# Performance work log

Measured on AMD Instinct MI355X. Metric: run time of the kernel, lower is better.

The kernel has to match this reference:

```python
import jax, jax.numpy as jnp
import numpy as np

N = 100000      # num nodes
E = 1600000     # random edges
F_IN = 128      # n_features
H1, H2 = 128, 64   # gnns_forward_hidden
FC1, C = 128, 10   # linears_hidden[-1], n_classes
M = 20000       # masked nodes
SLOPE = 0.2     # LeakyReLU negative slope (GATConv default)


def _glorot(key, shape):
    fan = shape[0]
    return jax.random.normal(key, shape, dtype=jnp.float32) / jnp.sqrt(jnp.float32(fan))


def setup_inputs() -> dict:
    key = jax.random.key(0)
    ks = jax.random.split(key, 16)
    x = jax.random.normal(ks[0], (N, F_IN), dtype=jnp.float32)
    edge_index = jax.random.randint(ks[1], (2, E), 0, N, dtype=jnp.int64)
    mask = jax.random.randint(ks[2], (M,), 0, N, dtype=jnp.int64)
    return {
        "x": x, "edge_index": edge_index, "mask": mask,
        # GAT layer 1: F_IN -> H1
        "W1": _glorot(ks[3], (F_IN, H1)),
        "a_src1": _glorot(ks[4], (H1,)), "a_dst1": _glorot(ks[5], (H1,)),
        "b1": jnp.zeros((H1,), jnp.float32),
        # GAT layer 2: H1 -> H2
        "W2": _glorot(ks[6], (H1, H2)),
        "a_src2": _glorot(ks[7], (H2,)), "a_dst2": _glorot(ks[8], (H2,)),
        "b2": jnp.zeros((H2,), jnp.float32),
        # FC head: H2 -> FC1 -> C
        "fc1_w": _glorot(ks[9], (H2, FC1)), "fc1_b": jnp.zeros((FC1,), jnp.float32),
        "fc2_w": _glorot(ks[10], (FC1, C)), "fc2_b": jnp.zeros((C,), jnp.float32),
    }


def _gat_layer(x, src, dst, W, a_src, a_dst, b):
    h = x @ W                                   # [N, F_out]
    alpha_s = h @ a_src                         # [N]
    alpha_d = h @ a_dst                         # [N]
    e = jax.nn.leaky_relu(alpha_s[src] + alpha_d[dst], SLOPE)  # [E+N]
    # segment softmax over incoming edges of each destination node
    m = jax.ops.segment_max(e, dst, num_segments=N)            # self-loops guarantee non-empty
    w = jnp.exp(e - m[dst])
    z = jax.ops.segment_sum(w, dst, num_segments=N)
    attn = w / z[dst]                           # [E+N]
    out = jax.ops.segment_sum(attn[:, None] * h[src], dst, num_segments=N)
    return out + b


def reference(x, edge_index, mask, W1, a_src1, a_dst1, b1, W2, a_src2, a_dst2, b2, fc1_w, fc1_b, fc2_w, fc2_b):
    loops = jnp.arange(N, dtype=edge_index.dtype)
    src = jnp.concatenate([edge_index[0], loops])   # random edges + self loops (norm_adj adds I)
    dst = jnp.concatenate([edge_index[1], loops])
    h = jax.nn.relu(_gat_layer(x, src, dst, W1, a_src1, a_dst1, b1))   # GATBlock 1 (eval: no dropout/BN)
    h = jax.nn.relu(_gat_layer(h, src, dst, W2, a_src2, a_dst2, b2))   # GATBlock 2
    hm = h[mask]                                    # x[mask] on last layer output
    z = jax.nn.relu(hm @ fc1_w + fc1_b)             # FCsBlock hidden layer
    return z @ fc2_w + fc2_b                        # logits [M, C]
```

## Files before the change

kernel.cpp:

```cpp
#include <hip/hip_runtime.h>
#include <hip/hip_bf16.h>

constexpr int kN    = 100000;
constexpr int kE    = 1600000;
constexpr int kTotE = kE + kN;
constexpr int kM    = 20000;
constexpr float kSlope = 0.2f;

constexpr int kNB   = (kN + 127) >> 7;
constexpr int kBCap = 3072;
constexpr int kEB   = 4096;
constexpr int kSB   = (kTotE + kEB - 1) / kEB;

typedef short short8  __attribute__((ext_vector_type(8)));
typedef float floatx4 __attribute__((ext_vector_type(4)));

__device__ __forceinline__ float bf2f(unsigned short u) {
  union { unsigned int i; float f; } v; v.i = ((unsigned int)u) << 16; return v.f;
}
__device__ __forceinline__ unsigned short f2bf(float f) {
  union { float f; unsigned int i; } v; v.f = f;
  unsigned int x = v.i;
  x += 0x7fffu + ((x >> 16) & 1u);
  return (unsigned short)(x >> 16);
}
__device__ __forceinline__ unsigned int packbf2(float lo, float hi) {
  __hip_bfloat162 h = __float22bfloat162_rn(float2{lo, hi});
  union { __hip_bfloat162 v; unsigned int u; } c; c.v = h; return c.u;
}
__device__ __forceinline__ unsigned short f2bf1(float f) {
  return (unsigned short)(packbf2(f, f) & 0xffffu);
}
__device__ __forceinline__ short8 pack8(float4 u, float4 v) {
  union { short8 s; unsigned int w[4]; } r;
  r.w[0] = packbf2(u.x, u.y); r.w[1] = packbf2(u.z, u.w);
  r.w[2] = packbf2(v.x, v.y); r.w[3] = packbf2(v.z, v.w);
  return r.s;
}

__global__ __launch_bounds__(256) void k_bscatter(const int* __restrict__ src,
                                                  const int* __restrict__ dst,
                                                  int* __restrict__ bucketCursor,
                                                  int* __restrict__ pairs) {
  __shared__ int hist[kNB];
  __shared__ int runBase[kNB];
  __shared__ int binCur[kNB];
  int b = blockIdx.x, t = threadIdx.x;
  for (int i = t; i < kNB; i += 256) hist[i] = 0;
  __syncthreads();
  int i0 = b * kEB;
#pragma unroll
  for (int k = 0; k < kEB / 256; ++k) {
    int i = i0 + t + k * 256;
    if (i < kTotE) {
      int d = (i < kE) ? dst[i] : (i - kE);
      atomicAdd(&hist[d >> 7], 1);
    }
  }
  __syncthreads();
  for (int i = t; i < kNB; i += 256) {
    int c = hist[i];
    int base = -1;
    if (c) {
      base = atomicAdd(&bucketCursor[i], c);
      if (base + c > kBCap) base = -1;
    }
    runBase[i] = base;
    binCur[i] = 0;
  }
  __syncthreads();
#pragma unroll
  for (int k = 0; k < kEB / 256; ++k) {
    int i = i0 + t + k * 256;
    if (i < kTotE) {
      int s, d;
      if (i < kE) { s = src[i]; d = dst[i]; }
      else        { s = d = i - kE; }
      int bin = d >> 7;
      int lp = atomicAdd(&binCur[bin], 1);
      int rb = runBase[bin];
      if (rb >= 0) pairs[(size_t)bin * kBCap + rb + lp] = ((d & 127) << 17) | s;
    }
  }
}

__global__ __launch_bounds__(1024) void k_bscan(const int* __restrict__ bucketCursor,
                                                int* __restrict__ colBase,
                                                int* __restrict__ rstart) {
  __shared__ int sh[1024];
  int t = threadIdx.x;
  int v = (t < kNB) ? min(bucketCursor[t], kBCap) : 0;
  sh[t] = v;
  __syncthreads();
  for (int off = 1; off < 1024; off <<= 1) {
    int u = (t >= off) ? sh[t - off] : 0;
    __syncthreads();
    sh[t] += u;
    __syncthreads();
  }
  if (t < kNB) colBase[t] = sh[t] - v;
  if (t == kNB - 1) { colBase[kNB] = sh[t]; rstart[kN] = sh[t]; }
}

__global__ __launch_bounds__(256) void k_bucket_csr(const int* __restrict__ pairs,
                                                    const int* __restrict__ bucketCursor,
                                                    const int* __restrict__ colBase,
                                                    int* __restrict__ rstart,
                                                    int* __restrict__ colidx) {
  __shared__ int pl[kBCap];
  __shared__ int colLDS[kBCap];
  __shared__ int nhist[128], nstart[128], ncur[128], scanbuf[128];
  int b = blockIdx.x, t = threadIdx.x;
  int cnt  = min(bucketCursor[b], kBCap);
  int base = colBase[b];
  if (t < 128) { nhist[t] = 0; ncur[t] = 0; }
  __syncthreads();
  for (int j = t; j < cnt; j += 256) {
    int p = pairs[(size_t)b * kBCap + j];
    pl[j] = p;
    atomicAdd(&nhist[(p >> 17) & 127], 1);
  }
  __syncthreads();
  if (t < 128) scanbuf[t] = nhist[t];
  __syncthreads();
  for (int off = 1; off < 128; off <<= 1) {
    int u = (t < 128 && t >= off) ? scanbuf[t - off] : 0;
    __syncthreads();
    if (t < 128) scanbuf[t] += u;
    __syncthreads();
  }
  if (t < 128) nstart[t] = scanbuf[t] - nhist[t];
  __syncthreads();
  int nodes = min(128, kN - b * 128);
  if (t < nodes) rstart[b * 128 + t] = base + nstart[t];
  for (int j = t; j < cnt; j += 256) {
    int p = pl[j];
    int nl = (p >> 17) & 127;
    int lp = atomicAdd(&ncur[nl], 1);
    colLDS[nstart[nl] + lp] = p & 0x1FFFF;
  }
  __syncthreads();
  for (int j = t; j < cnt; j += 256)
    colidx[base + j] = colLDS[j];
}

__global__ void k_wprep(const float* __restrict__ W,
                        unsigned short* __restrict__ Wf, int K, int Fo) {
  int idx = blockIdx.x * 256 + threadIdx.x;
  if (idx >= K * Fo) return;
  int j    = idx & 7;
  int lane = (idx >> 3) & 63;
  int t    = idx >> 9;
  int NT = Fo >> 4;
  int kt = t / NT, nt = t - kt * NT;
  int k = kt * 32 + ((lane >> 4) & 3) * 8 + j;
  int n = nt * 16 + (lane & 15);
  Wf[idx] = f2bf(W[k * Fo + n]);
}

__global__ __launch_bounds__(256) void k_gemm1(const float* __restrict__ x,
                                               const unsigned short* __restrict__ Wf,
                                               const float* __restrict__ asrc,
                                               const float* __restrict__ adst,
                                               unsigned short* __restrict__ h1,
                                               float* __restrict__ as, float* __restrict__ ad) {
  __shared__ unsigned short tile[4][16 * 128];
  int wave = threadIdx.x >> 6, lane = threadIdx.x & 63;
  int strip = blockIdx.x * 4 + wave;
  if (strip >= kN / 16) return;
  int r0 = strip * 16;
  int m = lane & 15, quad = lane >> 4;
  const float4* xf = (const float4*)(x + (size_t)(r0 + m) * 128);
  short8 a0 = pack8(xf[quad * 2 + 0],  xf[quad * 2 + 1]);
  short8 a1 = pack8(xf[quad * 2 + 8],  xf[quad * 2 + 9]);
  short8 a2 = pack8(xf[quad * 2 + 16], xf[quad * 2 + 17]);
  short8 a3 = pack8(xf[quad * 2 + 24], xf[quad * 2 + 25]);
  const short8* wf = (const short8*)Wf;
  floatx4 acc[8];
#pragma unroll
  for (int nt = 0; nt < 8; ++nt) acc[nt] = floatx4{0.f, 0.f, 0.f, 0.f};
#pragma unroll
  for (int nt = 0; nt < 8; ++nt) {
    acc[nt] = __builtin_amdgcn_mfma_f32_16x16x32_bf16(a0, wf[(0 * 8 + nt) * 64 + lane], acc[nt], 0, 0, 0);
    acc[nt] = __builtin_amdgcn_mfma_f32_16x16x32_bf16(a1, wf[(1 * 8 + nt) * 64 + lane], acc[nt], 0, 0, 0);
    acc[nt] = __builtin_amdgcn_mfma_f32_16x16x32_bf16(a2, wf[(2 * 8 + nt) * 64 + lane], acc[nt], 0, 0, 0);
    acc[nt] = __builtin_amdgcn_mfma_f32_16x16x32_bf16(a3, wf[(3 * 8 + nt) * 64 + lane], acc[nt], 0, 0, 0);
  }
#pragma unroll
  for (int reg = 0; reg < 4; ++reg) {
    float s = 0.f, d = 0.f;
#pragma unroll
    for (int nt = 0; nt < 8; ++nt) {
      float v = acc[nt][reg];
      s += v * asrc[nt * 16 + m];
      d += v * adst[nt * 16 + m];
    }
#pragma unroll
    for (int off = 1; off < 16; off <<= 1) { s += __shfl_xor(s, off); d += __shfl_xor(d, off); }
    if (m == 0) { as[r0 + quad * 4 + reg] = s; ad[r0 + quad * 4 + reg] = d; }
  }
  unsigned short* tw = tile[wave];
#pragma unroll
  for (int nt = 0; nt < 8; ++nt)
#pragma unroll
    for (int reg = 0; reg < 4; ++reg)
      tw[(quad * 4 + reg) * 128 + nt * 16 + m] = f2bf1(acc[nt][reg]);
  asm volatile("s_waitcnt lgkmcnt(0)" ::: "memory");
  const short8* tr = (const short8*)tw;
  short8* dstp = (short8*)(h1 + (size_t)r0 * 128);
#pragma unroll
  for (int sweep = 0; sweep < 4; ++sweep)
    dstp[sweep * 64 + lane] = tr[sweep * 64 + lane];
}

__global__ __launch_bounds__(256) void k_gemm2(const unsigned short* __restrict__ o1,
                                               const unsigned short* __restrict__ Wf,
                                               const float* __restrict__ asrc,
                                               const float* __restrict__ adst,
                                               unsigned short* __restrict__ h2,
                                               float* __restrict__ as, float* __restrict__ ad) {
  __shared__ unsigned short tile[4][16 * 64];
  int wave = threadIdx.x >> 6, lane = threadIdx.x & 63;
  int strip = blockIdx.x * 4 + wave;
  if (strip >= kN / 16) return;
  int r0 = strip * 16;
  int m = lane & 15, quad = lane >> 4;
  const short8* xs = (const short8*)(o1 + (size_t)(r0 + m) * 128);
  short8 a0 = xs[quad], a1 = xs[quad + 4], a2 = xs[quad + 8], a3 = xs[quad + 12];
  const short8* wf = (const short8*)Wf;
  floatx4 acc[4];
#pragma unroll
  for (int nt = 0; nt < 4; ++nt) acc[nt] = floatx4{0.f, 0.f, 0.f, 0.f};
#pragma unroll
  for (int nt = 0; nt < 4; ++nt) {
    acc[nt] = __builtin_amdgcn_mfma_f32_16x16x32_bf16(a0, wf[(0 * 4 + nt) * 64 + lane], acc[nt], 0, 0, 0);
    acc[nt] = __builtin_amdgcn_mfma_f32_16x16x32_bf16(a1, wf[(1 * 4 + nt) * 64 + lane], acc[nt], 0, 0, 0);
    acc[nt] = __builtin_amdgcn_mfma_f32_16x16x32_bf16(a2, wf[(2 * 4 + nt) * 64 + lane], acc[nt], 0, 0, 0);
    acc[nt] = __builtin_amdgcn_mfma_f32_16x16x32_bf16(a3, wf[(3 * 4 + nt) * 64 + lane], acc[nt], 0, 0, 0);
  }
#pragma unroll
  for (int reg = 0; reg < 4; ++reg) {
    float s = 0.f, d = 0.f;
#pragma unroll
    for (int nt = 0; nt < 4; ++nt) {
      float v = acc[nt][reg];
      s += v * asrc[nt * 16 + m];
      d += v * adst[nt * 16 + m];
    }
#pragma unroll
    for (int off = 1; off < 16; off <<= 1) { s += __shfl_xor(s, off); d += __shfl_xor(d, off); }
    if (m == 0) { as[r0 + quad * 4 + reg] = s; ad[r0 + quad * 4 + reg] = d; }
  }
  unsigned short* tw = tile[wave];
#pragma unroll
  for (int nt = 0; nt < 4; ++nt)
#pragma unroll
    for (int reg = 0; reg < 4; ++reg)
      tw[(quad * 4 + reg) * 64 + nt * 16 + m] = f2bf1(acc[nt][reg]);
  asm volatile("s_waitcnt lgkmcnt(0)" ::: "memory");
  const short8* tr = (const short8*)tw;
  short8* dstp = (short8*)(h2 + (size_t)r0 * 64);
#pragma unroll
  for (int sweep = 0; sweep < 2; ++sweep)
    dstp[sweep * 64 + lane] = tr[sweep * 64 + lane];
}

template <int F, bool MASKED>
__global__ __launch_bounds__(256) void k_agg(const unsigned short* __restrict__ h,
                                             const int* __restrict__ row_start,
                                             const int* __restrict__ col,
                                             const float* __restrict__ as,
                                             const float* __restrict__ ad,
                                             const float* __restrict__ bias,
                                             unsigned short* __restrict__ out,
                                             const int* __restrict__ maskIdx) {
  __shared__ int2 swb[4][64];
  int wave = threadIdx.x >> 6, lane = threadIdx.x & 63;
  int idx = blockIdx.x * 4 + wave;
  if (idx >= (MASKED ? kM : kN)) return;
  int n = MASKED ? maskIdx[idx] : idx;
  int nout = MASKED ? idx : n;
  int beg = row_start[n], end = row_start[n + 1];
  int deg = end - beg;
  float adn = ad[n];

  if (deg <= 64) {
    int j = beg + lane;
    int s = 0; float e = -1e30f;
    if (j < end) {
      s = col[j];
      float t = as[s] + adn;
      e = t > 0.f ? t : kSlope * t;
    }
    float mx = e;
#pragma unroll
    for (int off = 32; off; off >>= 1) mx = fmaxf(mx, __shfl_xor(mx, off));
    float w0 = __expf(e - mx);
    float l = w0;
#pragma unroll
    for (int off = 32; off; off >>= 1) l += __shfl_xor(l, off);
    float w = w0 * (1.f / l);
    swb[wave][lane] = int2{s, (int)__float_as_int(w)};
    asm volatile("s_waitcnt lgkmcnt(0)" ::: "memory");
    float a[8];
#pragma unroll
    for (int i = 0; i < 8; ++i) a[i] = 0.f;
    if (F == 128) {
      int quarter = lane >> 4, ql = lane & 15;
      int cnt4 = (deg + 3) & ~3;
      for (int k = 0; k < cnt4; k += 4) {
        int2 p = swb[wave][k + quarter];
        float ww = __int_as_float(p.y);
        uint4 v = *(const uint4*)(h + (size_t)p.x * 128 + ql * 8);
        a[0] += ww * bf2f((unsigned short)(v.x & 0xffffu));
        a[1] += ww * bf2f((unsigned short)(v.x >> 16));
        a[2] += ww * bf2f((unsigned short)(v.y & 0xffffu));
        a[3] += ww * bf2f((unsigned short)(v.y >> 16));
        a[4] += ww * bf2f((unsigned short)(v.z & 0xffffu));
        a[5] += ww * bf2f((unsigned short)(v.z >> 16));
        a[6] += ww * bf2f((unsigned short)(v.w & 0xffffu));
        a[7] += ww * bf2f((unsigned short)(v.w >> 16));
      }
#pragma unroll
      for (int i = 0; i < 8; ++i) {
        a[i] += __shfl_xor(a[i], 16);
        a[i] += __shfl_xor(a[i], 32);
      }
      if (quarter == 0) {
        float4 b0 = ((const float4*)bias)[ql * 2];
        float4 b1 = ((const float4*)bias)[ql * 2 + 1];
        uint4 pk;
        pk.x = packbf2(fmaxf(a[0] + b0.x, 0.f), fmaxf(a[1] + b0.y, 0.f));
        pk.y = packbf2(fmaxf(a[2] + b0.z, 0.f), fmaxf(a[3] + b0.w, 0.f));
        pk.z = packbf2(fmaxf(a[4] + b1.x, 0.f), fmaxf(a[5] + b1.y, 0.f));
        pk.w = packbf2(fmaxf(a[6] + b1.z, 0.f), fmaxf(a[7] + b1.w, 0.f));
        ((uint4*)(out + (size_t)nout * 128))[ql] = pk;
      }
    } else {
      int eighth = lane >> 3, el = lane & 7;
      int cnt8 = (deg + 7) & ~7;
      for (int k = 0; k < cnt8; k += 8) {
        int2 p = swb[wave][k + eighth];
        float ww = __int_as_float(p.y);
        uint4 v = *(const uint4*)(h + (size_t)p.x * 64 + el * 8);
        a[0] += ww * bf2f((unsigned short)(v.x & 0xffffu));
        a[1] += ww * bf2f((unsigned short)(v.x >> 16));
        a[2] += ww * bf2f((unsigned short)(v.y & 0xffffu));
        a[3] += ww * bf2f((unsigned short)(v.y >> 16));
        a[4] += ww * bf2f((unsigned short)(v.z & 0xffffu));
        a[5] += ww * bf2f((unsigned short)(v.z >> 16));
        a[6] += ww * bf2f((unsigned short)(v.w & 0xffffu));
        a[7] += ww * bf2f((unsigned short)(v.w >> 16));
      }
#pragma unroll
      for (int i = 0; i < 8; ++i) {
        a[i] += __shfl_xor(a[i], 8);
        a[i] += __shfl_xor(a[i], 16);
        a[i] += __shfl_xor(a[i], 32);
      }
      if (eighth == 0) {
        float4 b0 = ((const float4*)bias)[el * 2];
        float4 b1 = ((const float4*)bias)[el * 2 + 1];
        uint4 pk;
        pk.x = packbf2(fmaxf(a[0] + b0.x, 0.f), fmaxf(a[1] + b0.y, 0.f));
        pk.y = packbf2(fmaxf(a[2] + b0.z, 0.f), fmaxf(a[3] + b0.w, 0.f));
        pk.z = packbf2(fmaxf(a[4] + b1.x, 0.f), fmaxf(a[5] + b1.y, 0.f));
        pk.w = packbf2(fmaxf(a[6] + b1.z, 0.f), fmaxf(a[7] + b1.w, 0.f));
        ((uint4*)(out + (size_t)nout * 64))[el] = pk;
      }
    }
    return;
  }

  float m = -1e30f, l = 0.f;
  for (int j0 = beg; j0 < end; j0 += 64) {
    int j = j0 + lane;
    float e = -1e30f;
    if (j < end) {
      int s = col[j];
      float t = as[s] + adn;
      e = t > 0.f ? t : kSlope * t;
    }
    float cm = e;
#pragma unroll
    for (int off = 32; off; off >>= 1) cm = fmaxf(cm, __shfl_xor(cm, off));
    float w = __expf(e - cm);
    float cl = w;
#pragma unroll
    for (int off = 32; off; off >>= 1) cl += __shfl_xor(cl, off);
    float mn = fmaxf(m, cm);
    l = l * __expf(m - mn) + cl * __expf(cm - mn);
    m = mn;
  }
  float invl = 1.f / l;
  float a0 = 0.f, a1 = 0.f;
  int half = lane >> 5, hl = lane & 31;
  for (int j0 = beg; j0 < end; j0 += 64) {
    asm volatile("s_waitcnt lgkmcnt(0)" ::: "memory");
    int j = j0 + lane;
    if (j < end) {
      int s = col[j];
      float t = as[s] + adn;
      float e = t > 0.f ? t : kSlope * t;
      float w = __expf(e - m) * invl;
      swb[wave][lane] = int2{s, (int)__float_as_int(w)};
    }
    asm volatile("s_waitcnt lgkmcnt(0)" ::: "memory");
    int cntc = min(64, end - j0);
    if (F == 128) {
      for (int k = 0; k < cntc; ++k) {
        int2 p = swb[wave][k];
        float w = __int_as_float(p.y);
        unsigned int v = ((const unsigned int*)(h + (size_t)p.x * 128))[lane];
        a0 += w * bf2f((unsigned short)(v & 0xffffu));
        a1 += w * bf2f((unsigned short)(v >> 16));
      }
    } else {
      for (int k = 0; k < cntc; k += 2) {
        int kk = k + half;
        if (kk < cntc) {
          int2 p = swb[wave][kk];
          float w = __int_as_float(p.y);
          unsigned int v = ((const unsigned int*)(h + (size_t)p.x * 64))[hl];
          a0 += w * bf2f((unsigned short)(v & 0xffffu));
          a1 += w * bf2f((unsigned short)(v >> 16));
        }
      }
    }
  }
  if (F == 128) {
    float o0 = fmaxf(a0 + bias[2 * lane], 0.f);
    float o1 = fmaxf(a1 + bias[2 * lane + 1], 0.f);
    ((unsigned int*)(out + (size_t)nout * 128))[lane] = packbf2(o0, o1);
  } else {
    a0 += __shfl_xor(a0, 32);
    a1 += __shfl_xor(a1, 32);
    if (half == 0) {
      float o0 = fmaxf(a0 + bias[2 * hl], 0.f);
      float o1 = fmaxf(a1 + bias[2 * hl + 1], 0.f);
      ((unsigned int*)(out + (size_t)nout * 64))[hl] = packbf2(o0, o1);
    }
  }
}

__global__ __launch_bounds__(256) void k_fc1(const unsigned short* __restrict__ o2m,
                                             const unsigned short* __restrict__ Wf,
                                             const float* __restrict__ fc1b,
                                             unsigned short* __restrict__ z) {
  __shared__ unsigned short tile[4][16 * 128];
  int wave = threadIdx.x >> 6, lane = threadIdx.x & 63;
  int strip = blockIdx.x * 4 + wave;
  if (strip >= kM / 16) return;
  int r0 = strip * 16;
  int m = lane & 15, quad = lane >> 4;
  const short8* xs = (const short8*)(o2m + (size_t)(r0 + m) * 64);
  short8 a0 = xs[quad], a1 = xs[quad + 4];
  const short8* wf = (const short8*)Wf;
  floatx4 acc[8];
#pragma unroll
  for (int nt = 0; nt < 8; ++nt) acc[nt] = floatx4{0.f, 0.f, 0.f, 0.f};
#pragma unroll
  for (int nt = 0; nt < 8; ++nt) {
    acc[nt] = __builtin_amdgcn_mfma_f32_16x16x32_bf16(a0, wf[(0 * 8 + nt) * 64 + lane], acc[nt], 0, 0, 0);
    acc[nt] = __builtin_amdgcn_mfma_f32_16x16x32_bf16(a1, wf[(1 * 8 + nt) * 64 + lane], acc[nt], 0, 0, 0);
  }
  unsigned short* tw = tile[wave];
#pragma unroll
  for (int nt = 0; nt < 8; ++nt) {
    float bb = fc1b[nt * 16 + m];
#pragma unroll
    for (int reg = 0; reg < 4; ++reg)
      tw[(quad * 4 + reg) * 128 + nt * 16 + m] = f2bf1(fmaxf(acc[nt][reg] + bb, 0.f));
  }
  asm volatile("s_waitcnt lgkmcnt(0)" ::: "memory");
  const short8* tr = (const short8*)tw;
  short8* dstp = (short8*)(z + (size_t)r0 * 128);
#pragma unroll
  for (int sweep = 0; sweep < 4; ++sweep)
    dstp[sweep * 64 + lane] = tr[sweep * 64 + lane];
}

__global__ __launch_bounds__(256) void k_fc2(const unsigned short* __restrict__ z,
                                             const float* __restrict__ fc2w,
                                             const float* __restrict__ fc2b,
                                             float* __restrict__ out) {
  int wave = threadIdx.x >> 6, lane = threadIdx.x & 63;
  int c = lane & 15, q = lane >> 4;
  bool active = c < 10;
  float wreg[32];
#pragma unroll
  for (int i = 0; i < 32; ++i)
    wreg[i] = active ? fc2w[(q * 32 + i) * 10 + c] : 0.f;
  for (int row = blockIdx.x * 4 + wave; row < kM; row += gridDim.x * 4) {
    const uint2* zr = (const uint2*)(z + (size_t)row * 128);
    float acc = 0.f;
#pragma unroll
    for (int i = 0; i < 8; ++i) {
      uint2 v = zr[q * 8 + i];
      acc += bf2f((unsigned short)(v.x & 0xffffu)) * wreg[4 * i]
           + bf2f((unsigned short)(v.x >> 16))     * wreg[4 * i + 1]
           + bf2f((unsigned short)(v.y & 0xffffu)) * wreg[4 * i + 2]
           + bf2f((unsigned short)(v.y >> 16))     * wreg[4 * i + 3];
    }
    acc += __shfl_xor(acc, 16);
    acc += __shfl_xor(acc, 32);
    if (q == 0 && active) out[(size_t)row * 10 + c] = acc + fc2b[c];
  }
}

extern "C" void kernel_launch(void* const* d_in, const int* in_sizes, int n_in,
                              void* d_out, int out_size, void* d_ws, size_t ws_size,
                              hipStream_t stream) {
  const float* x     = (const float*)d_in[0];
  const int*   ei    = (const int*)d_in[1];
  const int*   mask  = (const int*)d_in[2];
  const float* W1    = (const float*)d_in[3];
  const float* asrc1 = (const float*)d_in[4];
  const float* adst1 = (const float*)d_in[5];
  const float* b1    = (const float*)d_in[6];
  const float* W2    = (const float*)d_in[7];
  const float* asrc2 = (const float*)d_in[8];
  const float* adst2 = (const float*)d_in[9];
  const float* b2    = (const float*)d_in[10];
  const float* fc1w  = (const float*)d_in[11];
  const float* fc1b  = (const float*)d_in[12];
  const float* fc2w  = (const float*)d_in[13];
  const float* fc2b  = (const float*)d_in[14];
  float* out = (float*)d_out;

  const int* esrc = ei;
  const int* edst = ei + kE;

  char* ws = (char*)d_ws;
  size_t off = 0;
  auto alloc = [&](size_t bytes) -> void* {
    void* p = ws + off;
    off = (off + bytes + 255) & ~(size_t)255;
    return p;
  };
  unsigned short* Wf1     = (unsigned short*)alloc(128 * 128 * 2);
  unsigned short* Wf2     = (unsigned short*)alloc(128 * 64 * 2);
  unsigned short* Wf3     = (unsigned short*)alloc(64 * 128 * 2);
  int*            rstart  = (int*)alloc((size_t)(kN + 1) * 4);
  int*            bcursor = (int*)alloc((size_t)kNB * 4);
  int*            colBase = (int*)alloc((size_t)(kNB + 1) * 4);
  float*          as1     = (float*)alloc((size_t)kN * 4);
  float*          ad1     = (float*)alloc((size_t)kN * 4);
  float*          as2     = (float*)alloc((size_t)kN * 4);
  float*          ad2     = (float*)alloc((size_t)kN * 4);
  int*            colidx  = (int*)alloc((size_t)kTotE * 4);
  int*            pairs   = (int*)alloc((size_t)kNB * kBCap * 4);
  unsigned short* zbuf    = (unsigned short*)alloc((size_t)kM * 128 * 2);
  unsigned short* h1      = (unsigned short*)alloc((size_t)kN * 128 * 2);
  unsigned short* o1      = (unsigned short*)alloc((size_t)kN * 128 * 2);
  unsigned short* h2  = h1;
  unsigned short* o2m = h1 + (size_t)kN * 64;
  (void)ws_size; (void)in_sizes; (void)n_in; (void)out_size;

  hipMemsetAsync(bcursor, 0, (size_t)kNB * 4, stream);
  k_bscatter<<<kSB, 256, 0, stream>>>(esrc, edst, bcursor, pairs);
  k_bscan<<<1, 1024, 0, stream>>>(bcursor, colBase, rstart);
  k_bucket_csr<<<kNB, 256, 0, stream>>>(pairs, bcursor, colBase, rstart, colidx);

  k_wprep<<<(128 * 128 + 255) / 256, 256, 0, stream>>>(W1, Wf1, 128, 128);
  k_wprep<<<(128 * 64 + 255) / 256, 256, 0, stream>>>(W2, Wf2, 128, 64);
  k_wprep<<<(64 * 128 + 255) / 256, 256, 0, stream>>>(fc1w, Wf3, 64, 128);

  const int gemmBlocks = (kN / 16 + 3) / 4;
  const int nodeBlocks = (kN + 3) / 4;
  const int maskBlocks = (kM + 3) / 4;

  k_gemm1<<<gemmBlocks, 256, 0, stream>>>(x, Wf1, asrc1, adst1, h1, as1, ad1);
  k_agg<128, false><<<nodeBlocks, 256, 0, stream>>>(h1, rstart, colidx, as1, ad1, b1, o1, nullptr);
  k_gemm2<<<gemmBlocks, 256, 0, stream>>>(o1, Wf2, asrc2, adst2, h2, as2, ad2);
  k_agg<64, true><<<maskBlocks, 256, 0, stream>>>(h2, rstart, colidx, as2, ad2, b2, o2m, mask);
  k_fc1<<<(kM / 16 + 3) / 4, 256, 0, stream>>>(o2m, Wf3, fc1b, zbuf);
  k_fc2<<<512, 256, 0, stream>>>(zbuf, fc2w, fc2b, out);
}
```

Before: 289.4 us.

## Fuse setup kernels, co-launch edge bucketing with GEMM1, drop scan, fuse FC head

Folds the cursor memset and the three weight-prep launches into a single setup kernel. Edge bucketing and the first GEMM now run as disjoint block ranges of one launch. The global bucket scan is dropped: CSR stays in the padded per-bucket layout, written in place into the pairs buffer, with a per-node degree array replacing row_start[n+1]. The aggregation kernels pull neighbour indices and weights by wave shuffle instead of an LDS staging buffer and issue two gathers per iteration, and FC1 and FC2 are fused so the hidden activations never go to global memory. The goal is fewer launches and less global traffic, at the cost of a padded CSR layout and a larger mixed-role kernel.

```diff
diff --git a/kernel.cpp b/kernel.cpp
--- a/kernel.cpp
+++ b/kernel.cpp
@@ -11,18 +11,13 @@
 constexpr int kBCap = 3072;
 constexpr int kEB   = 4096;
 constexpr int kSB   = (kTotE + kEB - 1) / kEB;
+constexpr int kG1B  = (kN / 16 + 3) / 4;
 
 typedef short short8  __attribute__((ext_vector_type(8)));
 typedef float floatx4 __attribute__((ext_vector_type(4)));
 
 __device__ __forceinline__ float bf2f(unsigned short u) {
   union { unsigned int i; float f; } v; v.i = ((unsigned int)u) << 16; return v.f;
-}
-__device__ __forceinline__ unsigned short f2bf(float f) {
-  union { float f; unsigned int i; } v; v.f = f;
-  unsigned int x = v.i;
-  x += 0x7fffu + ((x >> 16) & 1u);
-  return (unsigned short)(x >> 16);
 }
 __device__ __forceinline__ unsigned int packbf2(float lo, float hi) {
   __hip_bfloat162 h = __float22bfloat162_rn(float2{lo, hi});
@@ -38,116 +33,8 @@
   return r.s;
 }
 
-__global__ __launch_bounds__(256) void k_bscatter(const int* __restrict__ src,
-                                                  const int* __restrict__ dst,
-                                                  int* __restrict__ bucketCursor,
-                                                  int* __restrict__ pairs) {
-  __shared__ int hist[kNB];
-  __shared__ int runBase[kNB];
-  __shared__ int binCur[kNB];
-  int b = blockIdx.x, t = threadIdx.x;
-  for (int i = t; i < kNB; i += 256) hist[i] = 0;
-  __syncthreads();
-  int i0 = b * kEB;
-#pragma unroll
-  for (int k = 0; k < kEB / 256; ++k) {
-    int i = i0 + t + k * 256;
-    if (i < kTotE) {
-      int d = (i < kE) ? dst[i] : (i - kE);
-      atomicAdd(&hist[d >> 7], 1);
-    }
-  }
-  __syncthreads();
-  for (int i = t; i < kNB; i += 256) {
-    int c = hist[i];
-    int base = -1;
-    if (c) {
-      base = atomicAdd(&bucketCursor[i], c);
-      if (base + c > kBCap) base = -1;
-    }
-    runBase[i] = base;
-    binCur[i] = 0;
-  }
-  __syncthreads();
-#pragma unroll
-  for (int k = 0; k < kEB / 256; ++k) {
-    int i = i0 + t + k * 256;
-    if (i < kTotE) {
-      int s, d;
-      if (i < kE) { s = src[i]; d = dst[i]; }
-      else        { s = d = i - kE; }
-      int bin = d >> 7;
-      int lp = atomicAdd(&binCur[bin], 1);
-      int rb = runBase[bin];
-      if (rb >= 0) pairs[(size_t)bin * kBCap + rb + lp] = ((d & 127) << 17) | s;
-    }
-  }
-}
-
-__global__ __launch_bounds__(1024) void k_bscan(const int* __restrict__ bucketCursor,
-                                                int* __restrict__ colBase,
-                                                int* __restrict__ rstart) {
-  __shared__ int sh[1024];
-  int t = threadIdx.x;
-  int v = (t < kNB) ? min(bucketCursor[t], kBCap) : 0;
-  sh[t] = v;
-  __syncthreads();
-  for (int off = 1; off < 1024; off <<= 1) {
-    int u = (t >= off) ? sh[t - off] : 0;
-    __syncthreads();
-    sh[t] += u;
-    __syncthreads();
-  }
-  if (t < kNB) colBase[t] = sh[t] - v;
-  if (t == kNB - 1) { colBase[kNB] = sh[t]; rstart[kN] = sh[t]; }
-}
-
-__global__ __launch_bounds__(256) void k_bucket_csr(const int* __restrict__ pairs,
-                                                    const int* __restrict__ bucketCursor,
-                                                    const int* __restrict__ colBase,
-                                                    int* __restrict__ rstart,
-                                                    int* __restrict__ colidx) {
-  __shared__ int pl[kBCap];
-  __shared__ int colLDS[kBCap];
-  __shared__ int nhist[128], nstart[128], ncur[128], scanbuf[128];
-  int b = blockIdx.x, t = threadIdx.x;
-  int cnt  = min(bucketCursor[b], kBCap);
-  int base = colBase[b];
-  if (t < 128) { nhist[t] = 0; ncur[t] = 0; }
-  __syncthreads();
-  for (int j = t; j < cnt; j += 256) {
-    int p = pairs[(size_t)b * kBCap + j];
-    pl[j] = p;
-    atomicAdd(&nhist[(p >> 17) & 127], 1);
-  }
-  __syncthreads();
-  if (t < 128) scanbuf[t] = nhist[t];
-  __syncthreads();
-  for (int off = 1; off < 128; off <<= 1) {
-    int u = (t < 128 && t >= off) ? scanbuf[t - off] : 0;
-    __syncthreads();
-    if (t < 128) scanbuf[t] += u;
-    __syncthreads();
-  }
-  if (t < 128) nstart[t] = scanbuf[t] - nhist[t];
-  __syncthreads();
-  int nodes = min(128, kN - b * 128);
-  if (t < nodes) rstart[b * 128 + t] = base + nstart[t];
-  for (int j = t; j < cnt; j += 256) {
-    int p = pl[j];
-    int nl = (p >> 17) & 127;
-    int lp = atomicAdd(&ncur[nl], 1);
-    colLDS[nstart[nl] + lp] = p & 0x1FFFF;
-  }
-  __syncthreads();
-  for (int j = t; j < cnt; j += 256)
-    colidx[base + j] = colLDS[j];
-}
-
-__global__ void k_wprep(const float* __restrict__ W,
-                        unsigned short* __restrict__ Wf, int K, int Fo) {
-  int idx = blockIdx.x * 256 + threadIdx.x;
-  if (idx >= K * Fo) return;
+__device__ __forceinline__ void wprep1(int idx, const float* W, unsigned short* Wf,
+                                       int Fo) {
   int j    = idx & 7;
   int lane = (idx >> 3) & 63;
   int t    = idx >> 9;
@@ -155,18 +42,80 @@
   int kt = t / NT, nt = t - kt * NT;
   int k = kt * 32 + ((lane >> 4) & 3) * 8 + j;
   int n = nt * 16 + (lane & 15);
-  Wf[idx] = f2bf(W[k * Fo + n]);
-}
-
-__global__ __launch_bounds__(256) void k_gemm1(const float* __restrict__ x,
-                                               const unsigned short* __restrict__ Wf,
-                                               const float* __restrict__ asrc,
-                                               const float* __restrict__ adst,
-                                               unsigned short* __restrict__ h1,
-                                               float* __restrict__ as, float* __restrict__ ad) {
-  __shared__ unsigned short tile[4][16 * 128];
-  int wave = threadIdx.x >> 6, lane = threadIdx.x & 63;
-  int strip = blockIdx.x * 4 + wave;
+  Wf[idx] = f2bf1(W[k * Fo + n]);
+}
+
+__global__ __launch_bounds__(256) void k_setup(const float* __restrict__ W1,
+                                               const float* __restrict__ W2,
+                                               const float* __restrict__ fc1w,
+                                               unsigned short* __restrict__ Wf1,
+                                               unsigned short* __restrict__ Wf2,
+                                               unsigned short* __restrict__ Wf3,
+                                               int* __restrict__ bcursor) {
+  int gid = blockIdx.x * 256 + threadIdx.x;
+  if (gid < kNB) bcursor[gid] = 0;
+  if (gid < 16384)      wprep1(gid,          W1,   Wf1, 128);
+  else if (gid < 24576) wprep1(gid - 16384,  W2,   Wf2, 64);
+  else if (gid < 32768) wprep1(gid - 24576,  fc1w, Wf3, 128);
+}
+
+__global__ __launch_bounds__(256) void k_sg1(const int* __restrict__ esrc,
+                                             const int* __restrict__ edst,
+                                             int* __restrict__ bucketCursor,
+                                             int* __restrict__ pairs,
+                                             const float* __restrict__ x,
+                                             const unsigned short* __restrict__ Wf,
+                                             const float* __restrict__ asrc,
+                                             const float* __restrict__ adst,
+                                             unsigned short* __restrict__ h1,
+                                             float* __restrict__ as, float* __restrict__ ad) {
+  __shared__ int smemi[4096];
+  int t = threadIdx.x;
+  if (blockIdx.x < kSB) {
+    int* hist    = smemi;
+    int* runBase = smemi + kNB;
+    int* binCur  = smemi + 2 * kNB;
+    int b = blockIdx.x;
+    for (int i = t; i < kNB; i += 256) hist[i] = 0;
+    __syncthreads();
+    int i0 = b * kEB;
+#pragma unroll
+    for (int k = 0; k < kEB / 256; ++k) {
+      int i = i0 + t + k * 256;
+      if (i < kTotE) {
+        int d = (i < kE) ? edst[i] : (i - kE);
+        atomicAdd(&hist[d >> 7], 1);
+      }
+    }
+    __syncthreads();
+    for (int i = t; i < kNB; i += 256) {
+      int c = hist[i];
+      int base = -1;
+      if (c) {
+        base = atomicAdd(&bucketCursor[i], c);
+        if (base + c > kBCap) base = -1;
+      }
+      runBase[i] = base;
+      binCur[i] = 0;
+    }
+    __syncthreads();
+#pragma unroll
+    for (int k = 0; k < kEB / 256; ++k) {
+      int i = i0 + t + k * 256;
+      if (i < kTotE) {
+        int s, d;
+        if (i < kE) { s = esrc[i]; d = edst[i]; }
+        else        { s = d = i - kE; }
+        int bin = d >> 7;
+        int lp = atomicAdd(&binCur[bin], 1);
+        int rb = runBase[bin];
+        if (rb >= 0) pairs[(size_t)bin * kBCap + rb + lp] = ((d & 127) << 17) | s;
+      }
+    }
+    return;
+  }
+  int wave = t >> 6, lane = t & 63;
+  int strip = (blockIdx.x - kSB) * 4 + wave;
   if (strip >= kN / 16) return;
   int r0 = strip * 16;
   int m = lane & 15, quad = lane >> 4;
@@ -199,7 +148,7 @@
     for (int off = 1; off < 16; off <<= 1) { s += __shfl_xor(s, off); d += __shfl_xor(d, off); }
     if (m == 0) { as[r0 + quad * 4 + reg] = s; ad[r0 + quad * 4 + reg] = d; }
   }
-  unsigned short* tw = tile[wave];
+  unsigned short* tw = (unsigned short*)smemi + wave * 2048;
 #pragma unroll
   for (int nt = 0; nt < 8; ++nt)
 #pragma unroll
@@ -211,6 +160,50 @@
 #pragma unroll
   for (int sweep = 0; sweep < 4; ++sweep)
     dstp[sweep * 64 + lane] = tr[sweep * 64 + lane];
+}
+
+__global__ __launch_bounds__(256) void k_bucket_csr(int* __restrict__ pairs,
+                                                    const int* __restrict__ bucketCursor,
+                                                    int* __restrict__ rstart,
+                                                    int* __restrict__ degA) {
+  __shared__ int pl[kBCap];
+  __shared__ int colLDS[kBCap];
+  __shared__ int nhist[128], nstart[128], ncur[128], scanbuf[128];
+  int b = blockIdx.x, t = threadIdx.x;
+  int cnt  = min(bucketCursor[b], kBCap);
+  int base = b * kBCap;
+  if (t < 128) { nhist[t] = 0; ncur[t] = 0; }
+  __syncthreads();
+  for (int j = t; j < cnt; j += 256) {
+    int p = pairs[(size_t)base + j];
+    pl[j] = p;
+    atomicAdd(&nhist[(p >> 17) & 127], 1);
+  }
+  __syncthreads();
+  if (t < 128) scanbuf[t] = nhist[t];
+  __syncthreads();
+  for (int off = 1; off < 128; off <<= 1) {
+    int u = (t < 128 && t >= off) ? scanbuf[t - off] : 0;
+    __syncthreads();
+    if (t < 128) scanbuf[t] += u;
+    __syncthreads();
+  }
+  if (t < 128) nstart[t] = scanbuf[t] - nhist[t];
+  __syncthreads();
+  int nodes = min(128, kN - b * 128);
+  if (t < nodes) {
+    rstart[b * 128 + t] = base + nstart[t];
+    degA[b * 128 + t]   = nhist[t];
+  }
+  for (int j = t; j < cnt; j += 256) {
+    int p = pl[j];
+    int nl = (p >> 17) & 127;
+    int lp = atomicAdd(&ncur[nl], 1);
+    colLDS[nstart[nl] + lp] = p & 0x1FFFF;
+  }
+  __syncthreads();
+  for (int j = t; j < cnt; j += 256)
+    pairs[(size_t)base + j] = colLDS[j];
 }
 
 __global__ __launch_bounds__(256) void k_gemm2(const unsigned short* __restrict__ o1,
@@ -267,7 +260,8 @@
 
 template <int F, bool MASKED>
 __global__ __launch_bounds__(256) void k_agg(const unsigned short* __restrict__ h,
-                                             const int* __restrict__ row_start,
+                                             const int* __restrict__ rstart,
+                                             const int* __restrict__ degA,
                                              const int* __restrict__ col,
                                              const float* __restrict__ as,
                                              const float* __restrict__ ad,
@@ -280,14 +274,14 @@
   if (idx >= (MASKED ? kM : kN)) return;
   int n = MASKED ? maskIdx[idx] : idx;
   int nout = MASKED ? idx : n;
-  int beg = row_start[n], end = row_start[n + 1];
-  int deg = end - beg;
+  int beg = rstart[n];
+  int deg = degA[n];
   float adn = ad[n];
 
   if (deg <= 64) {
     int j = beg + lane;
     int s = 0; float e = -1e30f;
-    if (j < end) {
+    if (lane < deg) {
       s = col[j];
       float t = as[s] + adn;
       e = t > 0.f ? t : kSlope * t;
@@ -300,26 +294,34 @@
 #pragma unroll
     for (int off = 32; off; off >>= 1) l += __shfl_xor(l, off);
     float w = w0 * (1.f / l);
-    swb[wave][lane] = int2{s, (int)__float_as_int(w)};
-    asm volatile("s_waitcnt lgkmcnt(0)" ::: "memory");
     float a[8];
 #pragma unroll
     for (int i = 0; i < 8; ++i) a[i] = 0.f;
     if (F == 128) {
       int quarter = lane >> 4, ql = lane & 15;
-      int cnt4 = (deg + 3) & ~3;
-      for (int k = 0; k < cnt4; k += 4) {
-        int2 p = swb[wave][k + quarter];
-        float ww = __int_as_float(p.y);
-        uint4 v = *(const uint4*)(h + (size_t)p.x * 128 + ql * 8);
-        a[0] += ww * bf2f((unsigned short)(v.x & 0xffffu));
-        a[1] += ww * bf2f((unsigned short)(v.x >> 16));
-        a[2] += ww * bf2f((unsigned short)(v.y & 0xffffu));
-        a[3] += ww * bf2f((unsigned short)(v.y >> 16));
-        a[4] += ww * bf2f((unsigned short)(v.z & 0xffffu));
-        a[5] += ww * bf2f((unsigned short)(v.z >> 16));
-        a[6] += ww * bf2f((unsigned short)(v.w & 0xffffu));
-        a[7] += ww * bf2f((unsigned short)(v.w >> 16));
+      int cnt8 = (deg + 7) & ~7;
+      for (int k = 0; k < cnt8; k += 8) {
+        int i1 = k + quarter, i2 = i1 + 4;
+        int   s1 = __shfl(s, i1), s2 = __shfl(s, i2);
+        float w1 = __shfl(w, i1), w2 = __shfl(w, i2);
+        uint4 v1 = *(const uint4*)(h + (size_t)s1 * 128 + ql * 8);
+        uint4 v2 = *(const uint4*)(h + (size_t)s2 * 128 + ql * 8);
+        a[0] += w1 * bf2f((unsigned short)(v1.x & 0xffffu));
+        a[1] += w1 * bf2f((unsigned short)(v1.x >> 16));
+        a[2] += w1 * bf2f((unsigned short)(v1.y & 0xffffu));
+        a[3] += w1 * bf2f((unsigned short)(v1.y >> 16));
+        a[4] += w1 * bf2f((unsigned short)(v1.z & 0xffffu));
+        a[5] += w1 * bf2f((unsigned short)(v1.z >> 16));
+        a[6] += w1 * bf2f((unsigned short)(v1.w & 0xffffu));
+        a[7] += w1 * bf2f((unsigned short)(v1.w >> 16));
+        a[0] += w2 * bf2f((unsigned short)(v2.x & 0xffffu));
+        a[1] += w2 * bf2f((unsigned short)(v2.x >> 16));
+        a[2] += w2 * bf2f((unsigned short)(v2.y & 0xffffu));
+        a[3] += w2 * bf2f((unsigned short)(v2.y >> 16));
+        a[4] += w2 * bf2f((unsigned short)(v2.z & 0xffffu));
+        a[5] += w2 * bf2f((unsigned short)(v2.z >> 16));
+        a[6] += w2 * bf2f((unsigned short)(v2.w & 0xffffu));
+        a[7] += w2 * bf2f((unsigned short)(v2.w >> 16));
       }
 #pragma unroll
       for (int i = 0; i < 8; ++i) {
@@ -338,19 +340,29 @@
       }
     } else {
       int eighth = lane >> 3, el = lane & 7;
-      int cnt8 = (deg + 7) & ~7;
-      for (int k = 0; k < cnt8; k += 8) {
-        int2 p = swb[wave][k + eighth];
-        float ww = __int_as_float(p.y);
-        uint4 v = *(const uint4*)(h + (size_t)p.x * 64 + el * 8);
-        a[0] += ww * bf2f((unsigned short)(v.x & 0xffffu));
-        a[1] += ww * bf2f((unsigned short)(v.x >> 16));
-        a[2] += ww * bf2f((unsigned short)(v.y & 0xffffu));
-        a[3] += ww * bf2f((unsigned short)(v.y >> 16));
-        a[4] += ww * bf2f((unsigned short)(v.z & 0xffffu));
-        a[5] += ww * bf2f((unsigned short)(v.z >> 16));
-        a[6] += ww * bf2f((unsigned short)(v.w & 0xffffu));
-        a[7] += ww * bf2f((unsigned short)(v.w >> 16));
+      int cnt16 = (deg + 15) & ~15;
+      for (int k = 0; k < cnt16; k += 16) {
+        int i1 = k + eighth, i2 = i1 + 8;
+        int   s1 = __shfl(s, i1), s2 = __shfl(s, i2);
+        float w1 = __shfl(w, i1), w2 = __shfl(w, i2);
+        uint4 v1 = *(const uint4*)(h + (size_t)s1 * 64 + el * 8);
+        uint4 v2 = *(const uint4*)(h + (size_t)s2 * 64 + el * 8);
+        a[0] += w1 * bf2f((unsigned short)(v1.x & 0xffffu));
+        a[1] += w1 * bf2f((unsigned short)(v1.x >> 16));
+        a[2] += w1 * bf2f((unsigned short)(v1.y & 0xffffu));
+        a[3] += w1 * bf2f((unsigned short)(v1.y >> 16));
+        a[4] += w1 * bf2f((unsigned short)(v1.z & 0xffffu));
+        a[5] += w1 * bf2f((unsigned short)(v1.z >> 16));
+        a[6] += w1 * bf2f((unsigned short)(v1.w & 0xffffu));
+        a[7] += w1 * bf2f((unsigned short)(v1.w >> 16));
+        a[0] += w2 * bf2f((unsigned short)(v2.x & 0xffffu));
+        a[1] += w2 * bf2f((unsigned short)(v2.x >> 16));
+        a[2] += w2 * bf2f((unsigned short)(v2.y & 0xffffu));
+        a[3] += w2 * bf2f((unsigned short)(v2.y >> 16));
+        a[4] += w2 * bf2f((unsigned short)(v2.z & 0xffffu));
+        a[5] += w2 * bf2f((unsigned short)(v2.z >> 16));
+        a[6] += w2 * bf2f((unsigned short)(v2.w & 0xffffu));
+        a[7] += w2 * bf2f((unsigned short)(v2.w >> 16));
       }
 #pragma unroll
       for (int i = 0; i < 8; ++i) {
@@ -372,6 +384,7 @@
     return;
   }
 
+  int end = beg + deg;
   float m = -1e30f, l = 0.f;
   for (int j0 = beg; j0 < end; j0 += 64) {
     int j = j0 + lane;
@@ -443,10 +456,12 @@
   }
 }
 
-__global__ __launch_bounds__(256) void k_fc1(const unsigned short* __restrict__ o2m,
-                                             const unsigned short* __restrict__ Wf,
-                                             const float* __restrict__ fc1b,
-                                             unsigned short* __restrict__ z) {
+__global__ __launch_bounds__(256) void k_fc(const unsigned short* __restrict__ o2m,
+                                            const unsigned short* __restrict__ Wf,
+                                            const float* __restrict__ fc1b,
+                                            const float* __restrict__ fc2w,
+                                            const float* __restrict__ fc2b,
+                                            float* __restrict__ out) {
   __shared__ unsigned short tile[4][16 * 128];
   int wave = threadIdx.x >> 6, lane = threadIdx.x & 63;
   int strip = blockIdx.x * 4 + wave;
@@ -473,38 +488,27 @@
       tw[(quad * 4 + reg) * 128 + nt * 16 + m] = f2bf1(fmaxf(acc[nt][reg] + bb, 0.f));
   }
   asm volatile("s_waitcnt lgkmcnt(0)" ::: "memory");
-  const short8* tr = (const short8*)tw;
-  short8* dstp = (short8*)(z + (size_t)r0 * 128);
-#pragma unroll
-  for (int sweep = 0; sweep < 4; ++sweep)
-    dstp[sweep * 64 + lane] = tr[sweep * 64 + lane];
-}
-
-__global__ __launch_bounds__(256) void k_fc2(const unsigned short* __restrict__ z,
-                                             const float* __restrict__ fc2w,
-                                             const float* __restrict__ fc2b,
-                                             float* __restrict__ out) {
-  int wave = threadIdx.x >> 6, lane = threadIdx.x & 63;
   int c = lane & 15, q = lane >> 4;
   bool active = c < 10;
   float wreg[32];
 #pragma unroll
   for (int i = 0; i < 32; ++i)
     wreg[i] = active ? fc2w[(q * 32 + i) * 10 + c] : 0.f;
-  for (int row = blockIdx.x * 4 + wave; row < kM; row += gridDim.x * 4) {
-    const uint2* zr = (const uint2*)(z + (size_t)row * 128);
-    float acc = 0.f;
+  float bc = active ? fc2b[c] : 0.f;
+  for (int r = 0; r < 16; ++r) {
+    const uint2* zr = (const uint2*)(tw + r * 128 + q * 32);
+    float acc2 = 0.f;
 #pragma unroll
     for (int i = 0; i < 8; ++i) {
-      uint2 v = zr[q * 8 + i];
-      acc += bf2f((unsigned short)(v.x & 0xffffu)) * wreg[4 * i]
-           + bf2f((unsigned short)(v.x >> 16))     * wreg[4 * i + 1]
-           + bf2f((unsigned short)(v.y & 0xffffu)) * wreg[4 * i + 2]
-           + bf2f((unsigned short)(v.y >> 16))     * wreg[4 * i + 3];
-    }
-    acc += __shfl_xor(acc, 16);
-    acc += __shfl_xor(acc, 32);
-    if (q == 0 && active) out[(size_t)row * 10 + c] = acc + fc2b[c];
+      uint2 v = zr[i];
+      acc2 += bf2f((unsigned short)(v.x & 0xffffu)) * wreg[4 * i]
+            + bf2f((unsigned short)(v.x >> 16))     * wreg[4 * i + 1]
+            + bf2f((unsigned short)(v.y & 0xffffu)) * wreg[4 * i + 2]
+            + bf2f((unsigned short)(v.y >> 16))     * wreg[4 * i + 3];
+    }
+    acc2 += __shfl_xor(acc2, 16);
+    acc2 += __shfl_xor(acc2, 32);
+    if (q == 0 && active) out[(size_t)(r0 + r) * 10 + c] = acc2 + bc;
   }
 }
 
@@ -541,39 +545,31 @@
   unsigned short* Wf1     = (unsigned short*)alloc(128 * 128 * 2);
   unsigned short* Wf2     = (unsigned short*)alloc(128 * 64 * 2);
   unsigned short* Wf3     = (unsigned short*)alloc(64 * 128 * 2);
-  int*            rstart  = (int*)alloc((size_t)(kN + 1) * 4);
+  int*            rstart  = (int*)alloc((size_t)kN * 4);
+  int*            degA    = (int*)alloc((size_t)kN * 4);
   int*            bcursor = (int*)alloc((size_t)kNB * 4);
-  int*            colBase = (int*)alloc((size_t)(kNB + 1) * 4);
   float*          as1     = (float*)alloc((size_t)kN * 4);
   float*          ad1     = (float*)alloc((size_t)kN * 4);
   float*          as2     = (float*)alloc((size_t)kN * 4);
   float*          ad2     = (float*)alloc((size_t)kN * 4);
-  int*            colidx  = (int*)alloc((size_t)kTotE * 4);
   int*            pairs   = (int*)alloc((size_t)kNB * kBCap * 4);
-  unsigned short* zbuf    = (unsigned short*)alloc((size_t)kM * 128 * 2);
   unsigned short* h1      = (unsigned short*)alloc((size_t)kN * 128 * 2);
   unsigned short* o1      = (unsigned short*)alloc((size_t)kN * 128 * 2);
   unsigned short* h2  = h1;
   unsigned short* o2m = h1 + (size_t)kN * 64;
   (void)ws_size; (void)in_sizes; (void)n_in; (void)out_size;
 
-  hipMemsetAsync(bcursor, 0, (size_t)kNB * 4, stream);
-  k_bscatter<<<kSB, 256, 0, stream>>>(esrc, edst, bcursor, pairs);
-  k_bscan<<<1, 1024, 0, stream>>>(bcursor, colBase, rstart);
-  k_bucket_csr<<<kNB, 256, 0, stream>>>(pairs, bcursor, colBase, rstart, colidx);
-
-  k_wprep<<<(128 * 128 + 255) / 256, 256, 0, stream>>>(W1, Wf1, 128, 128);
-  k_wprep<<<(128 * 64 + 255) / 256, 256, 0, stream>>>(W2, Wf2, 128, 64);
-  k_wprep<<<(64 * 128 + 255) / 256, 256, 0, stream>>>(fc1w, Wf3, 64, 128);
-
-  const int gemmBlocks = (kN / 16 + 3) / 4;
   const int nodeBlocks = (kN + 3) / 4;
   const int maskBlocks = (kM + 3) / 4;
 
-  k_gemm1<<<gemmBlocks, 256, 0, stream>>>(x, Wf1, asrc1, adst1, h1, as1, ad1);
-  k_agg<128, false><<<nodeBlocks, 256, 0, stream>>>(h1, rstart, colidx, as1, ad1, b1, o1, nullptr);
-  k_gemm2<<<gemmBlocks, 256, 0, stream>>>(o1, Wf2, asrc2, adst2, h2, as2, ad2);
-  k_agg<64, true><<<maskBlocks, 256, 0, stream>>>(h2, rstart, colidx, as2, ad2, b2, o2m, mask);
-  k_fc1<<<(kM / 16 + 3) / 4, 256, 0, stream>>>(o2m, Wf3, fc1b, zbuf);
-  k_fc2<<<512, 256, 0, stream>>>(zbuf, fc2w, fc2b, out);
-}
+  k_setup<<<128, 256, 0, stream>>>(W1, W2, fc1w, Wf1, Wf2, Wf3, bcursor);
+  k_sg1<<<kSB + kG1B, 256, 0, stream>>>(esrc, edst, bcursor, pairs,
+                                        x, Wf1, asrc1, adst1, h1, as1, ad1);
+  k_bucket_csr<<<kNB, 256, 0, stream>>>(pairs, bcursor, rstart, degA);
+  k_agg<128, false><<<nodeBlocks, 256, 0, stream>>>(h1, rstart, degA, pairs,
+                                                    as1, ad1, b1, o1, nullptr);
+  k_gemm2<<<kG1B, 256, 0, stream>>>(o1, Wf2, asrc2, adst2, h2, as2, ad2);
+  k_agg<64, true><<<maskBlocks, 256, 0, stream>>>(h2, rstart, degA, pairs,
+                                                  as2, ad2, b2, o2m, mask);
+  k_fc<<<(kM / 16 + 3) / 4, 256, 0, stream>>>(o2m, Wf3, fc1b, fc2w, fc2b, out);
+}
```

Result: faster. 259.2 us (-10.4%).
